# Kernel tuning notes

Measured on AMD Instinct MI355X. Metric: run time of the kernel, lower is better.

The kernel has to match this reference:

```python
import jax, jax.numpy as jnp
import numpy as np

# Model dims (see init_kwargs)
B, S, D = 2, 2048, 2048          # batch, seq, hidden
H, HD = 16, 128                  # heads, head_dim (= ND + RD)
ND, RD = 64, 64                  # nope dim, rope dim per head
R = 512                          # kv lora rank
THETA = 10000.0


def _rotate_half(x):
    # interleaved rotation: pairs (x0,x1) -> (-x1, x0)
    x1 = x[..., ::2]
    x2 = x[..., 1::2]
    return jnp.stack((-x2, x1), axis=-1).reshape(x.shape)


def apply_rope(x, positions):
    # x: [..., seq, dim]
    dim = x.shape[-1]
    freqs = 1.0 / THETA ** (jnp.arange(0, dim, 2, dtype=x.dtype) / dim)  # [dim/2]
    angles = positions.astype(x.dtype)[:, None] * freqs                  # [seq, dim/2]
    cos = jnp.repeat(jnp.cos(angles), 2, axis=-1)[None, None]            # [1,1,seq,dim]
    sin = jnp.repeat(jnp.sin(angles), 2, axis=-1)[None, None]
    return x * cos + _rotate_half(x) * sin


def setup_inputs() -> dict:
    key = jax.random.key(0)
    ks = jax.random.split(key, 7)
    def lin(k, out_f, in_f):  # torch Linear convention: weight [out, in]
        return jax.random.normal(k, (out_f, in_f), dtype=jnp.float32) * (in_f ** -0.5)
    return {
        "x": jax.random.normal(ks[0], (B, S, D), dtype=jnp.float32),
        "wq": lin(ks[1], D, D),
        "w_kv_down": lin(ks[2], R, D),
        "w_k_up": lin(ks[3], H * ND, R),
        "w_k_rope": lin(ks[4], RD, D),
        "w_v_up": lin(ks[5], D, R),
        "wo": lin(ks[6], D, D),
    }


def reference(x, wq, w_kv_down, w_k_up, w_k_rope, w_v_up, wo):
    b, s, _ = x.shape
    pos = jnp.arange(s)
    scale = 1.0 / np.sqrt(HD).astype(np.float32)

    # queries: [b,H,s,HD] split into nope/rope parts, rope applied per head
    q = (x @ wq.T).reshape(b, s, H, HD).transpose(0, 2, 1, 3)
    q_nope = q[..., :ND]
    q_rope = apply_rope(q[..., ND:], pos)

    # compressed kv latent: [b,s,R]
    c_kv = x @ w_kv_down.T
    k_nope = (c_kv @ w_k_up.T).reshape(b, s, H, ND).transpose(0, 2, 1, 3)  # [b,H,s,ND]
    k_rope = apply_rope((x @ w_k_rope.T)[:, None], pos)[:, 0]             # [b,s,RD], shared across heads
    v = (c_kv @ w_v_up.T).reshape(b, s, H, HD).transpose(0, 2, 1, 3)      # [b,H,s,HD]

    # decomposed scores: nope part (per head) + rope part (shared k)
    scores = jnp.einsum('bhqd,bhkd->bhqk', q_nope, k_nope)
    scores = scores + jnp.einsum('bhqd,bkd->bhqk', q_rope, k_rope)
    scores = scores * scale

    causal = jnp.tril(jnp.ones((s, s), dtype=bool))
    scores = jnp.where(causal[None, None], scores, jnp.finfo(scores.dtype).min)
    attn = jax.nn.softmax(scores, axis=-1)

    out = jnp.einsum('bhqk,bhkd->bhqd', attn, v)
    out = out.transpose(0, 2, 1, 3).reshape(b, s, D)
    return out @ wo.T
```

## Files before the change

kernel.cpp:

```cpp
#include <hip/hip_runtime.h>
#include <stdint.h>


typedef unsigned short u16;
typedef __bf16 bf16x8 __attribute__((ext_vector_type(8)));
typedef float f32x4 __attribute__((ext_vector_type(4)));

#define QLD 2816

__device__ __forceinline__ float bf2f(u16 u) {
    union { unsigned int i; float f; } x; x.i = ((unsigned int)u) << 16; return x.f;
}
__device__ __forceinline__ u16 f2bf(float f) {
    union { float f; unsigned int i; } x; x.f = f;
    unsigned int r = x.i + 0x7fffu + ((x.i >> 16) & 1u);
    return (u16)(r >> 16);
}
__device__ __forceinline__ void store_c(u16* p, float v)  { *p = f2bf(v); }
__device__ __forceinline__ void store_c(float* p, float v){ *p = v; }

#define GLOBAL_AS __attribute__((address_space(1)))
#define LDS_AS    __attribute__((address_space(3)))
__device__ __forceinline__ void gl_lds16(const void* g, void* l) {
    __builtin_amdgcn_global_load_lds((GLOBAL_AS const void*)g, (LDS_AS void*)l, 16, 0, 0);
}

#if __has_builtin(__builtin_amdgcn_exp2f)
__device__ __forceinline__ float exp2fast(float x) { return __builtin_amdgcn_exp2f(x); }
#else
__device__ __forceinline__ float exp2fast(float x) { return __expf(x * 0.6931471805599453f); }
#endif

template<int CTRL>
__device__ __forceinline__ float fmax_dpp(float v) {
    int s = __builtin_bit_cast(int, v);
    int t = __builtin_amdgcn_update_dpp(s, s, CTRL, 0xF, 0xF, true);
    return fmaxf(v, __builtin_bit_cast(float, t));
}
__device__ __forceinline__ float rowmax16(float v) {
    v = fmax_dpp<0xB1>(v);
    v = fmax_dpp<0x4E>(v);
    v = fmax_dpp<0x124>(v);
    v = fmax_dpp<0x128>(v);
    return v;
}

__global__ void convert_in(const float* __restrict__ src, u16* __restrict__ dst,
                           int n8) {
    int i = blockIdx.x * 256 + threadIdx.x;
    if (i >= n8) return;
    const float4* s = (const float4*)src;
    float4 v0 = s[2*i], v1 = s[2*i + 1];
    union { u16 u[8]; uint4 v; } o;
    o.u[0] = f2bf(v0.x); o.u[1] = f2bf(v0.y); o.u[2] = f2bf(v0.z); o.u[3] = f2bf(v0.w);
    o.u[4] = f2bf(v1.x); o.u[5] = f2bf(v1.y); o.u[6] = f2bf(v1.z); o.u[7] = f2bf(v1.w);
    *((uint4*)(dst + 8*i)) = o.v;
}

template<int BM, int BN, int EPI, typename CT>
__global__ __launch_bounds__((BM/64)*(BN/64)*64)
void gemm_bt(const u16* __restrict__ A, const u16* __restrict__ W,
             CT* __restrict__ C, int M, int N, int K,
             int lda, int ldw, int ldc) {
    constexpr int BK = 32;
    constexpr int NWAVE = (BM/64)*(BN/64);
    constexpr int NT = NWAVE * 64;
    __shared__ u16 As[BM*BK];
    __shared__ u16 Bs[BN*BK];
    const int tid  = threadIdx.x;
    const int lane = tid & 63, l15 = lane & 15, quad = lane >> 4;
    const int wave = tid >> 6;
    const int wm = wave % (BM/64);
    const int wn = wave / (BM/64);
    const int bm = blockIdx.y * BM;
    const int bn = blockIdx.x * BN;

    const f32x4 fzero = {0.f, 0.f, 0.f, 0.f};
    f32x4 acc[4][4];
    #pragma unroll
    for (int i = 0; i < 4; ++i)
        #pragma unroll
        for (int j = 0; j < 4; ++j) acc[i][j] = fzero;

    const size_t Ab = (size_t)lda * 2;
    const size_t Wb = (size_t)ldw * 2;

    for (int k0 = 0; k0 < K; k0 += BK) {
        #pragma unroll
        for (int i = 0; i < (BM*64)/(NT*16); ++i) {
            int o = (tid + i*NT) * 16;
            int row = o >> 6, colb = o & 63;
            gl_lds16((const char*)A + (size_t)(bm + row)*Ab + (size_t)k0*2 + colb,
                     (char*)As + o);
        }
        #pragma unroll
        for (int i = 0; i < (BN*64)/(NT*16); ++i) {
            int o = (tid + i*NT) * 16;
            int row = o >> 6, colb = o & 63;
            gl_lds16((const char*)W + (size_t)(bn + row)*Wb + (size_t)k0*2 + colb,
                     (char*)Bs + o);
        }
        __syncthreads();

        bf16x8 af[4], bfv[4];
        #pragma unroll
        for (int mt = 0; mt < 4; ++mt)
            af[mt] = *reinterpret_cast<const bf16x8*>(&As[(wm*64 + mt*16 + l15)*BK + quad*8]);
        #pragma unroll
        for (int nt = 0; nt < 4; ++nt)
            bfv[nt] = *reinterpret_cast<const bf16x8*>(&Bs[(wn*64 + nt*16 + l15)*BK + quad*8]);
        #pragma unroll
        for (int mt = 0; mt < 4; ++mt)
            #pragma unroll
            for (int nt = 0; nt < 4; ++nt)
                acc[mt][nt] = __builtin_amdgcn_mfma_f32_16x16x32_bf16(
                    af[mt], bfv[nt], acc[mt][nt], 0, 0, 0);
        __syncthreads();
    }

    #pragma unroll
    for (int mt = 0; mt < 4; ++mt)
        #pragma unroll
        for (int nt = 0; nt < 4; ++nt)
            #pragma unroll
            for (int r = 0; r < 4; ++r) {
                int gm = bm + wm*64 + mt*16 + quad*4 + r;
                int gn = bn + wn*64 + nt*16 + l15;
                size_t ci;
                if (EPI == 1) ci = (size_t)gm*ldc + ((gn >> 6)*128 + (gn & 63));
                else          ci = (size_t)gm*ldc + gn;
                store_c(&C[ci], acc[mt][nt][r]);
            }
}

template<typename CT>
__global__ __launch_bounds__(512, 2)
void gemm256(const u16* __restrict__ A, const u16* __restrict__ W,
             CT* __restrict__ C, int K, int lda, int ldw, int ldc) {
    __shared__ u16 lds[4][16384];
    const int tid  = threadIdx.x;
    const int lane = tid & 63, l15 = lane & 15, quad = lane >> 4;
    const int wave = tid >> 6;
    const int wr = wave >> 2, wc = wave & 3;
    const int bm = blockIdx.y * 256;
    const int bn = blockIdx.x * 256;

    const int R = tid >> 2, slot = tid & 3;
    const int k16 = slot ^ ((R >> 1) & 3);
    const u16* asrc = A + (size_t)(bm + R) * lda + k16 * 8;
    const u16* bsrc = W + (size_t)(bn + R) * ldw + k16 * 8;
    const size_t astep = (size_t)128 * lda;
    const size_t bstep = (size_t)128 * ldw;

    #define STAGE256(st, bi) { \
        const u16* a0_ = asrc + (size_t)(st) * 32; \
        const u16* b0_ = bsrc + (size_t)(st) * 32; \
        gl_lds16(a0_,         &lds[bi][tid * 8]); \
        gl_lds16(a0_ + astep, &lds[bi][(tid + 512) * 8]); \
        gl_lds16(b0_,         &lds[bi][(tid + 1024) * 8]); \
        gl_lds16(b0_ + bstep, &lds[bi][(tid + 1536) * 8]); \
    }

    const f32x4 fzero = {0.f, 0.f, 0.f, 0.f};
    f32x4 acc[8][4];
    #pragma unroll
    for (int i = 0; i < 8; ++i)
        #pragma unroll
        for (int j = 0; j < 4; ++j) acc[i][j] = fzero;

    const int aswz = (quad ^ ((l15 >> 1) & 3)) * 8;

    const int nst = K >> 5;
    STAGE256(0, 0)
    STAGE256(1, 1)
    STAGE256(2, 2)
    asm volatile("s_waitcnt vmcnt(8)" ::: "memory");
    __builtin_amdgcn_s_barrier();

    for (int t = 0; t < nst; ++t) {
        const u16* buf = lds[t & 3];
        bf16x8 af[8], bfv[4];
        #pragma unroll
        for (int mf = 0; mf < 8; ++mf)
            af[mf] = *reinterpret_cast<const bf16x8*>(
                &buf[(wr*128 + mf*16 + l15)*32 + aswz]);
        #pragma unroll
        for (int nf = 0; nf < 4; ++nf)
            bfv[nf] = *reinterpret_cast<const bf16x8*>(
                &buf[8192 + (wc*64 + nf*16 + l15)*32 + aswz]);
        int st = t + 3; if (st > nst - 1) st = nst - 1;
        STAGE256(st, (t + 3) & 3)
        __builtin_amdgcn_s_setprio(1);
        #pragma unroll
        for (int mf = 0; mf < 8; ++mf)
            #pragma unroll
            for (int nf = 0; nf < 4; ++nf)
                acc[mf][nf] = __builtin_amdgcn_mfma_f32_16x16x32_bf16(
                    af[mf], bfv[nf], acc[mf][nf], 0, 0, 0);
        __builtin_amdgcn_s_setprio(0);
        asm volatile("s_waitcnt vmcnt(8) lgkmcnt(0)" ::: "memory");
        __builtin_amdgcn_sched_barrier(0);
        __builtin_amdgcn_s_barrier();
        __builtin_amdgcn_sched_barrier(0);
    }
    #undef STAGE256

    #pragma unroll
    for (int mf = 0; mf < 8; ++mf)
        #pragma unroll
        for (int nf = 0; nf < 4; ++nf)
            #pragma unroll
            for (int r = 0; r < 4; ++r) {
                int gm = bm + wr*128 + mf*16 + quad*4 + r;
                int gn = bn + wc*64 + nf*16 + l15;
                store_c(&C[(size_t)gm * ldc + gn], acc[mf][nf][r]);
            }
}

__global__ void rope_q(u16* __restrict__ qcat) {
    int idx = blockIdx.x * 256 + threadIdx.x;
    int i = idx & 31, r = idx >> 5;
    int pos = r & 2047;
    float freq = powf(10000.0f, -(float)i * (1.0f/32.0f));
    float ang  = (float)pos * freq;
    float s = sinf(ang), c = cosf(ang);
    u16* row = qcat + (size_t)r * QLD + 64 + 2*i;
    #pragma unroll
    for (int h = 0; h < 16; ++h) {
        unsigned int* p = (unsigned int*)(row + h*128);
        unsigned int v = *p;
        float x0 = bf2f((u16)(v & 0xffffu)), x1 = bf2f((u16)(v >> 16));
        unsigned int lo = f2bf(x0*c - x1*s);
        unsigned int hi = f2bf(x1*c + x0*s);
        *p = lo | (hi << 16);
    }
}

__global__ void rope_kr_bcast(const u16* __restrict__ qcat, u16* __restrict__ keff) {
    int idx = blockIdx.x * 256 + threadIdx.x;
    int i = idx & 31, r = idx >> 5;
    int pos = r & 2047;
    float freq = powf(10000.0f, -(float)i * (1.0f/32.0f));
    float ang  = (float)pos * freq;
    float s = sinf(ang), c = cosf(ang);
    const u16* p = qcat + (size_t)r * QLD + 2048 + 2*i;
    float x0 = bf2f(p[0]), x1 = bf2f(p[1]);
    union { u16 u[2]; unsigned int w; } o;
    o.u[0] = f2bf(x0*c - x1*s);
    o.u[1] = f2bf(x1*c + x0*s);
    unsigned int* base = (unsigned int*)(keff + (size_t)r*2048 + 64 + 2*i);
    #pragma unroll
    for (int h = 0; h < 16; ++h) base[h*64] = o.w;
}

__global__ __launch_bounds__(256, 3)
void attn_kernel(u16* __restrict__ qcat, const u16* __restrict__ KE,
                 const u16* __restrict__ VT) {
    constexpr int S = 2048;
    const int L = (int)blockIdx.y * 16 + (int)blockIdx.x;
    const int xcd = L & 7, j = L >> 3;
    const int bh   = xcd * 4 + (j & 3);
    const int pair = j >> 2;
    const int b = bh >> 4, h = bh & 15;

    __shared__ u16 Ks[64*128];
    __shared__ u16 Vs[128*64];
    __shared__ u16 Ps[64*68];

    const int tid  = threadIdx.x;
    const int lane = tid & 63, l15 = lane & 15, quad = lane >> 4;
    const int wave = tid >> 6;

    const u16* ksrc[4];
    const u16* vsrc[4];
    #pragma unroll
    for (int i = 0; i < 4; ++i) {
        int g = tid + i*256;
        {
            int r = g >> 4, slot = g & 15, cg = slot ^ (r & 15);
            ksrc[i] = KE + (size_t)(b*S + r)*2048 + h*128 + cg*8;
        }
        {
            int d = g >> 3, slot = g & 7, cg = slot ^ (d & 7);
            vsrc[i] = VT + (size_t)(h*128 + d)*4096 + (size_t)(b*S) + cg*8;
        }
    }

    bf16x8 kreg[4], vreg[4];
    #pragma unroll
    for (int i = 0; i < 4; ++i) {
        kreg[i] = *reinterpret_cast<const bf16x8*>(ksrc[i]);
        vreg[i] = *reinterpret_cast<const bf16x8*>(vsrc[i]);
    }

    union { u16 u[8]; bf16x8 v; } onesu;
    #pragma unroll
    for (int i = 0; i < 8; ++i) onesu.u[i] = 0x3f80;
    const bf16x8 ones = onesu.v;

    const f32x4 fzero = {0.f, 0.f, 0.f, 0.f};
    const float NEG = -1e30f;
    const float KLOG = 0.12751739f;
    const float THR = 8.0f;

    __bf16* PsB = reinterpret_cast<__bf16*>(Ps);

    for (int half = 0; half < 2; ++half) {
        const int qt = half ? pair : 31 - pair;
        const int nkt = qt + 1;

        u16* qbase = qcat + (size_t)(b*S + qt*64) * QLD + h*128;
        bf16x8 aq[4];
        #pragma unroll
        for (int ks = 0; ks < 4; ++ks)
            aq[ks] = *reinterpret_cast<const bf16x8*>(
                qbase + (size_t)(wave*16 + l15)*QLD + ks*32 + quad*8);

        float m2[4]  = {NEG, NEG, NEG, NEG};
        float l_i[4] = {0.f, 0.f, 0.f, 0.f};
        f32x4 oacc[8];
        #pragma unroll
        for (int i = 0; i < 8; ++i) oacc[i] = fzero;

        const int qrow0 = qt*64 + wave*16 + quad*4;

        for (int kt = 0; kt < nkt; ++kt) {
            const bool is_last = (kt == nkt - 1);
            #pragma unroll
            for (int i = 0; i < 4; ++i) {
                *reinterpret_cast<bf16x8*>(&Ks[(tid + i*256) * 8]) = kreg[i];
                *reinterpret_cast<bf16x8*>(&Vs[(tid + i*256) * 8]) = vreg[i];
            }
            {
                int ktn = (kt + 1 < nkt) ? kt + 1 : 0;
                #pragma unroll
                for (int i = 0; i < 4; ++i) {
                    kreg[i] = *reinterpret_cast<const bf16x8*>(ksrc[i] + (size_t)ktn*(64*2048));
                    vreg[i] = *reinterpret_cast<const bf16x8*>(vsrc[i] + (size_t)ktn*64);
                }
            }
            __syncthreads();

            f32x4 sfr[4];
            #pragma unroll
            for (int nt = 0; nt < 4; ++nt) {
                f32x4 s = fzero;
                int n = nt*16 + l15;
                #pragma unroll
                for (int ks = 0; ks < 4; ++ks) {
                    int c = ks*4 + quad;
                    bf16x8 bk = *reinterpret_cast<const bf16x8*>(&Ks[n*128 + ((c ^ l15) * 8)]);
                    s = __builtin_amdgcn_mfma_f32_16x16x32_bf16(aq[ks], bk, s, 0, 0, 0);
                }
                sfr[nt] = s;
            }
            if (is_last) {
                #pragma unroll
                for (int nt = 0; nt < 4; ++nt) {
                    int kg = kt*64 + nt*16 + l15;
                    #pragma unroll
                    for (int r = 0; r < 4; ++r)
                        if (kg > qrow0 + r) sfr[nt][r] = NEG;
                }
            }
            float rm[4];
            #pragma unroll
            for (int r = 0; r < 4; ++r) {
                rm[r] = fmaxf(fmaxf(sfr[0][r], sfr[1][r]), fmaxf(sfr[2][r], sfr[3][r]));
                rm[r] = rowmax16(rm[r]);
            }
            float c2[4];
            int need = 0;
            #pragma unroll
            for (int r = 0; r < 4; ++r) {
                c2[r] = rm[r] * KLOG;
                need |= (c2[r] > m2[r] + THR) ? 1 : 0;
            }
            if (__any(need)) {
                float alpha[4];
                #pragma unroll
                for (int r = 0; r < 4; ++r) {
                    float mn = fmaxf(m2[r], c2[r]);
                    alpha[r] = exp2fast(m2[r] - mn);
                    m2[r] = mn;
                    l_i[r] *= alpha[r];
                }
                #pragma unroll
                for (int i = 0; i < 8; ++i)
                    #pragma unroll
                    for (int r = 0; r < 4; ++r)
                        oacc[i][r] *= alpha[r];
            }
            float pf[4][4];
            #pragma unroll
            for (int nt = 0; nt < 4; ++nt)
                #pragma unroll
                for (int r = 0; r < 4; ++r)
                    pf[nt][r] = exp2fast(__builtin_fmaf(sfr[nt][r], KLOG, -m2[r]));

            #pragma unroll
            for (int nt = 0; nt < 4; ++nt) {
                int base = (wave*16 + quad*4)*68 + nt*16 + l15;
                #pragma unroll
                for (int r = 0; r < 4; ++r)
                    PsB[base + r*68] = (__bf16)pf[nt][r];
            }

            f32x4 lfr = fzero;
            #pragma unroll
            for (int ks = 0; ks < 2; ++ks) {
                bf16x8 pa = *reinterpret_cast<const bf16x8*>(
                    &Ps[(wave*16 + l15)*68 + ks*32 + quad*8]);
                lfr = __builtin_amdgcn_mfma_f32_16x16x32_bf16(pa, ones, lfr, 0, 0, 0);
                #pragma unroll
                for (int ntv = 0; ntv < 8; ++ntv) {
                    int c = ks*4 + quad;
                    bf16x8 bv = *reinterpret_cast<const bf16x8*>(
                        &Vs[(ntv*16 + l15)*64 + ((c ^ (l15 & 7)) * 8)]);
                    oacc[ntv] = __builtin_amdgcn_mfma_f32_16x16x32_bf16(pa, bv, oacc[ntv], 0, 0, 0);
                }
            }
            #pragma unroll
            for (int r = 0; r < 4; ++r) l_i[r] += lfr[r];
            __syncthreads();
        }

        #pragma unroll
        for (int r = 0; r < 4; ++r) {
            float inv = 1.0f / l_i[r];
            int qrow = wave*16 + quad*4 + r;
            #pragma unroll
            for (int ntv = 0; ntv < 8; ++ntv) {
                int d = ntv*16 + l15;
                qbase[(size_t)qrow*QLD + d] = f2bf(oacc[ntv][r] * inv);
            }
        }
    }
}

extern "C" void kernel_launch(void* const* d_in, const int* in_sizes, int n_in,
                              void* d_out, int out_size, void* d_ws, size_t ws_size,
                              hipStream_t stream) {
    (void)in_sizes; (void)n_in; (void)out_size; (void)ws_size;
    float* out = (float*)d_out;
    char* ws = (char*)d_ws;

    u16* xc     = (u16*)(ws);
    u16* qcat   = (u16*)(ws + 16777216);
    u16* keff   = (u16*)(ws + 39845888);
    u16* wqcat  = (u16*)(ws + 56623104);
    u16* kupc   = (u16*)(ws + 68157440);
    u16* vupc   = (u16*)(ws + 69206016);
    u16* vT     = xc;
    u16* woc    = wqcat;

    convert_in<<<(1048576+255)/256, 256, 0, stream>>>((const float*)d_in[0], xc, 1048576);
    convert_in<<<( 524288+255)/256, 256, 0, stream>>>((const float*)d_in[1], wqcat, 524288);
    convert_in<<<(  16384+255)/256, 256, 0, stream>>>((const float*)d_in[4], wqcat + 2048*2048, 16384);
    convert_in<<<( 131072+255)/256, 256, 0, stream>>>((const float*)d_in[2], wqcat + 2112*2048, 131072);
    convert_in<<<(  65536+255)/256, 256, 0, stream>>>((const float*)d_in[3], kupc, 65536);
    convert_in<<<( 131072+255)/256, 256, 0, stream>>>((const float*)d_in[5], vupc, 131072);

    gemm256<u16><<<dim3(11, 16), 512, 0, stream>>>(
        xc, wqcat, qcat, 2048, 2048, 2048, QLD);

    convert_in<<<(524288+255)/256, 256, 0, stream>>>((const float*)d_in[6], woc, 524288);

    rope_q<<<512, 256, 0, stream>>>(qcat);
    rope_kr_bcast<<<512, 256, 0, stream>>>(qcat, keff);

    gemm_bt<128,128,1><<<dim3(8, 32), 256, 0, stream>>>(
        qcat + 2112, kupc, keff, 4096, 1024, 512, QLD, 512, 2048);

    gemm256<u16><<<dim3(16, 8), 512, 0, stream>>>(
        vupc, qcat + 2112, vT, 512, 512, QLD, 4096);

    attn_kernel<<<dim3(16, 32), 256, 0, stream>>>(qcat, keff, vT);

    gemm256<float><<<dim3(8, 16), 512, 0, stream>>>(
        qcat, woc, out, 2048, QLD, 2048, 2048);
}
```

Before: 347.1 us.

## Halve attention query tile and add 128-row GEMM variant for more blocks

```diff
diff --git a/kernel.cpp b/kernel.cpp
--- a/kernel.cpp
+++ b/kernel.cpp
@@ -217,6 +217,90 @@
             }
 }
 
+template<typename CT>
+__global__ __launch_bounds__(512, 4)
+void gemm128(const u16* __restrict__ A, const u16* __restrict__ W,
+             CT* __restrict__ C, int K, int lda, int ldw, int ldc) {
+    __shared__ u16 lds[3][12288];
+    const int tid  = threadIdx.x;
+    const int lane = tid & 63, l15 = lane & 15, quad = lane >> 4;
+    const int wave = tid >> 6;
+    const int wr = wave >> 2, wc = wave & 3;
+    const int bm = blockIdx.y * 128;
+    const int bn = blockIdx.x * 256;
+
+    const int R = tid >> 2, slot = tid & 3;
+    const int k16 = slot ^ ((R >> 1) & 3);
+    const u16* asrc = A + (size_t)(bm + R) * lda + k16 * 8;
+    const u16* bsrc = W + (size_t)(bn + R) * ldw + k16 * 8;
+    const size_t bstep = (size_t)128 * ldw;
+
+    #define STAGE128(st, bi) { \
+        const u16* a0_ = asrc + (size_t)(st) * 32; \
+        const u16* b0_ = bsrc + (size_t)(st) * 32; \
+        gl_lds16(a0_,         &lds[bi][tid * 8]); \
+        gl_lds16(b0_,         &lds[bi][(tid + 512) * 8]); \
+        gl_lds16(b0_ + bstep, &lds[bi][(tid + 1024) * 8]); \
+    }
+
+    const f32x4 fzero = {0.f, 0.f, 0.f, 0.f};
+    f32x4 acc[4][4];
+    #pragma unroll
+    for (int i = 0; i < 4; ++i)
+        #pragma unroll
+        for (int j = 0; j < 4; ++j) acc[i][j] = fzero;
+
+    const int aswz = (quad ^ ((l15 >> 1) & 3)) * 8;
+
+    const int nst = K >> 5;
+    STAGE128(0, 0)
+    STAGE128(1, 1)
+    asm volatile("s_waitcnt vmcnt(3)" ::: "memory");
+    __builtin_amdgcn_s_barrier();
+
+    int b0 = 0, bs = 2;
+    for (int t = 0; t < nst; ++t) {
+        const u16* buf = lds[b0];
+        bf16x8 af[4], bfv[4];
+        #pragma unroll
+        for (int mf = 0; mf < 4; ++mf)
+            af[mf] = *reinterpret_cast<const bf16x8*>(
+                &buf[(wr*64 + mf*16 + l15)*32 + aswz]);
+        #pragma unroll
+        for (int nf = 0; nf < 4; ++nf)
+            bfv[nf] = *reinterpret_cast<const bf16x8*>(
+                &buf[4096 + (wc*64 + nf*16 + l15)*32 + aswz]);
+        int st = t + 2; if (st > nst - 1) st = nst - 1;
+        STAGE128(st, bs)
+        __builtin_amdgcn_s_setprio(1);
+        #pragma unroll
+        for (int mf = 0; mf < 4; ++mf)
+            #pragma unroll
+            for (int nf = 0; nf < 4; ++nf)
+                acc[mf][nf] = __builtin_amdgcn_mfma_f32_16x16x32_bf16(
+                    af[mf], bfv[nf], acc[mf][nf], 0, 0, 0);
+        __builtin_amdgcn_s_setprio(0);
+        asm volatile("s_waitcnt vmcnt(3) lgkmcnt(0)" ::: "memory");
+        __builtin_amdgcn_sched_barrier(0);
+        __builtin_amdgcn_s_barrier();
+        __builtin_amdgcn_sched_barrier(0);
+        b0 = (b0 == 2) ? 0 : b0 + 1;
+        bs = (bs == 2) ? 0 : bs + 1;
+    }
+    #undef STAGE128
+
+    #pragma unroll
+    for (int mf = 0; mf < 4; ++mf)
+        #pragma unroll
+        for (int nf = 0; nf < 4; ++nf)
+            #pragma unroll
+            for (int r = 0; r < 4; ++r) {
+                int gm = bm + wr*64 + mf*16 + quad*4 + r;
+                int gn = bn + wc*64 + nf*16 + l15;
+                store_c(&C[(size_t)gm * ldc + gn], acc[mf][nf][r]);
+            }
+}
+
 __global__ void rope_q(u16* __restrict__ qcat) {
     int idx = blockIdx.x * 256 + threadIdx.x;
     int i = idx & 31, r = idx >> 5;
@@ -253,11 +337,11 @@
     for (int h = 0; h < 16; ++h) base[h*64] = o.w;
 }
 
-__global__ __launch_bounds__(256, 3)
+__global__ __launch_bounds__(128, 2)
 void attn_kernel(u16* __restrict__ qcat, const u16* __restrict__ KE,
                  const u16* __restrict__ VT) {
     constexpr int S = 2048;
-    const int L = (int)blockIdx.y * 16 + (int)blockIdx.x;
+    const int L = (int)blockIdx.y * 32 + (int)blockIdx.x;
     const int xcd = L & 7, j = L >> 3;
     const int bh   = xcd * 4 + (j & 3);
     const int pair = j >> 2;
@@ -265,17 +349,17 @@
 
     __shared__ u16 Ks[64*128];
     __shared__ u16 Vs[128*64];
-    __shared__ u16 Ps[64*68];
+    __shared__ u16 Ps[32*68];
 
     const int tid  = threadIdx.x;
     const int lane = tid & 63, l15 = lane & 15, quad = lane >> 4;
     const int wave = tid >> 6;
 
-    const u16* ksrc[4];
-    const u16* vsrc[4];
-    #pragma unroll
-    for (int i = 0; i < 4; ++i) {
-        int g = tid + i*256;
+    const u16* ksrc[8];
+    const u16* vsrc[8];
+    #pragma unroll
+    for (int i = 0; i < 8; ++i) {
+        int g = tid + i*128;
         {
             int r = g >> 4, slot = g & 15, cg = slot ^ (r & 15);
             ksrc[i] = KE + (size_t)(b*S + r)*2048 + h*128 + cg*8;
@@ -286,9 +370,9 @@
         }
     }
 
-    bf16x8 kreg[4], vreg[4];
-    #pragma unroll
-    for (int i = 0; i < 4; ++i) {
+    bf16x8 kreg[8], vreg[8];
+    #pragma unroll
+    for (int i = 0; i < 8; ++i) {
         kreg[i] = *reinterpret_cast<const bf16x8*>(ksrc[i]);
         vreg[i] = *reinterpret_cast<const bf16x8*>(vsrc[i]);
     }
@@ -306,10 +390,10 @@
     __bf16* PsB = reinterpret_cast<__bf16*>(Ps);
 
     for (int half = 0; half < 2; ++half) {
-        const int qt = half ? pair : 31 - pair;
-        const int nkt = qt + 1;
-
-        u16* qbase = qcat + (size_t)(b*S + qt*64) * QLD + h*128;
+        const int qt = half ? pair : 63 - pair;
+        const int nkt = (qt >> 1) + 1;
+
+        u16* qbase = qcat + (size_t)(b*S + qt*32) * QLD + h*128;
         bf16x8 aq[4];
         #pragma unroll
         for (int ks = 0; ks < 4; ++ks)
@@ -322,19 +406,19 @@
         #pragma unroll
         for (int i = 0; i < 8; ++i) oacc[i] = fzero;
 
-        const int qrow0 = qt*64 + wave*16 + quad*4;
+        const int qrow0 = qt*32 + wave*16 + quad*4;
 
         for (int kt = 0; kt < nkt; ++kt) {
             const bool is_last = (kt == nkt - 1);
             #pragma unroll
-            for (int i = 0; i < 4; ++i) {
-                *reinterpret_cast<bf16x8*>(&Ks[(tid + i*256) * 8]) = kreg[i];
-                *reinterpret_cast<bf16x8*>(&Vs[(tid + i*256) * 8]) = vreg[i];
+            for (int i = 0; i < 8; ++i) {
+                *reinterpret_cast<bf16x8*>(&Ks[(tid + i*128) * 8]) = kreg[i];
+                *reinterpret_cast<bf16x8*>(&Vs[(tid + i*128) * 8]) = vreg[i];
             }
             {
                 int ktn = (kt + 1 < nkt) ? kt + 1 : 0;
                 #pragma unroll
-                for (int i = 0; i < 4; ++i) {
+                for (int i = 0; i < 8; ++i) {
                     kreg[i] = *reinterpret_cast<const bf16x8*>(ksrc[i] + (size_t)ktn*(64*2048));
                     vreg[i] = *reinterpret_cast<const bf16x8*>(vsrc[i] + (size_t)ktn*64);
                 }
@@ -472,11 +556,11 @@
     gemm_bt<128,128,1><<<dim3(8, 32), 256, 0, stream>>>(
         qcat + 2112, kupc, keff, 4096, 1024, 512, QLD, 512, 2048);
 
-    gemm256<u16><<<dim3(16, 8), 512, 0, stream>>>(
+    gemm128<u16><<<dim3(16, 16), 512, 0, stream>>>(
         vupc, qcat + 2112, vT, 512, 512, QLD, 4096);
 
-    attn_kernel<<<dim3(16, 32), 256, 0, stream>>>(qcat, keff, vT);
-
-    gemm256<float><<<dim3(8, 16), 512, 0, stream>>>(
+    attn_kernel<<<dim3(32, 32), 128, 0, stream>>>(qcat, keff, vT);
+
+    gemm128<float><<<dim3(8, 32), 512, 0, stream>>>(
         qcat, woc, out, 2048, QLD, 2048, 2048);
 }
```

Result: no change. 342.1 us (-1.4%).
